# Kernel optimization log

Hardware: AMD Instinct MI355X
Metric: run time of the kernel (lower is better)

The kernel has to match this reference:

```python
import jax, jax.numpy as jnp
import numpy as np

# dims
B, FIN, FOUT = 4, 64, 32
FMID = min(FIN, FOUT)          # fmiddle
NCLS, NH = 4, 64               # num_classes, SPADE nhidden
S = 32                         # D = H = W
EPS = 1e-5


def conv3d(x, w, b=None, pad=1):
    # x: [N,C,D,H,W], w: [O,I,kd,kh,kw]
    out = jax.lax.conv_general_dilated(
        x, w, window_strides=(1, 1, 1), padding=[(pad, pad)] * 3,
        dimension_numbers=('NCDHW', 'OIDHW', 'NCDHW'))
    if b is not None:
        out = out + b[None, :, None, None, None]
    return out


def instance_norm(x):
    # per-sample, per-channel over spatial dims (InstanceNorm3d, affine=False)
    mu = x.mean(axis=(2, 3, 4), keepdims=True)
    var = x.var(axis=(2, 3, 4), keepdims=True)
    return (x - mu) * jax.lax.rsqrt(var + EPS)


def spade(x, y, Ws, Bs, Wg, Bg, Wb, Bb):
    # x: [B,C,D,H,W]; param stacks have leading num_classes dim; y routes per sample.
    normalized = instance_norm(x)
    ws, bs, wg, bg, wb, bb = Ws[y], Bs[y], Wg[y], Bg[y], Wb[y], Bb[y]

    def one(xi, wsi, bsi, wgi, bgi, wbi, bbi):
        xi = xi[None]  # [1,C,D,H,W]
        actv = jax.nn.relu(conv3d(xi, wsi, bsi))
        gamma = conv3d(actv, wgi, bgi)[0]
        beta = conv3d(actv, wbi, bbi)[0]
        return gamma, beta

    gamma, beta = jax.vmap(one)(x, ws, bs, wg, bg, wb, bb)
    return normalized * (1.0 + gamma) + beta


def _lrelu(t):
    return jax.nn.leaky_relu(t, 0.2)


def setup_inputs() -> dict:
    key = jax.random.key(0)
    ks = jax.random.split(key, 24)
    sc = 0.05
    inp = {
        'x': jax.random.normal(ks[0], (B, FIN, S, S, S), jnp.float32),
        'y': jax.random.randint(ks[1], (B,), 0, NCLS, jnp.int64
                                if jax.config.jax_enable_x64 else jnp.int32),
        # SPADE norm_0 stacks: label_nc = norm_nc = FIN
        's0_ws': jax.random.normal(ks[2], (NCLS, NH, FIN, 3, 3, 3), jnp.float32) * sc,
        's0_bs': jnp.zeros((NCLS, NH), jnp.float32),
        's0_wg': jax.random.normal(ks[3], (NCLS, FIN, NH, 3, 3, 3), jnp.float32) * sc,
        's0_bg': jnp.zeros((NCLS, FIN), jnp.float32),
        's0_wb': jax.random.normal(ks[4], (NCLS, FIN, NH, 3, 3, 3), jnp.float32) * sc,
        's0_bb': jnp.zeros((NCLS, FIN), jnp.float32),
        # SPADE norm_1 stacks: label_nc = norm_nc = FMID
        's1_ws': jax.random.normal(ks[5], (NCLS, NH, FMID, 3, 3, 3), jnp.float32) * sc,
        's1_bs': jnp.zeros((NCLS, NH), jnp.float32),
        's1_wg': jax.random.normal(ks[6], (NCLS, FMID, NH, 3, 3, 3), jnp.float32) * sc,
        's1_bg': jnp.zeros((NCLS, FMID), jnp.float32),
        's1_wb': jax.random.normal(ks[7], (NCLS, FMID, NH, 3, 3, 3), jnp.float32) * sc,
        's1_bb': jnp.zeros((NCLS, FMID), jnp.float32),
        # resnet convs
        'conv0_w': jax.random.normal(ks[8], (FMID, FIN, 3, 3, 3), jnp.float32) * sc,
        'conv0_b': jnp.zeros((FMID,), jnp.float32),
        'conv1_w': jax.random.normal(ks[9], (FOUT, FMID, 3, 3, 3), jnp.float32) * sc,
        'conv1_b': jnp.zeros((FOUT,), jnp.float32),
        'convs_w': jax.random.normal(ks[10], (FOUT, FIN, 1, 1, 1), jnp.float32) * sc,
    }
    return inp


def reference(x, y, s0_ws, s0_bs, s0_wg, s0_bg, s0_wb, s0_bb,
              s1_ws, s1_bs, s1_wg, s1_bg, s1_wb, s1_bb,
              conv0_w, conv0_b, conv1_w, conv1_b, convs_w):
    x_s = conv3d(x, convs_w, None, pad=0)  # learned shortcut (fin != fout, no bias)
    dx = conv3d(_lrelu(spade(x, y, s0_ws, s0_bs, s0_wg, s0_bg, s0_wb, s0_bb)),
                conv0_w, conv0_b)
    dx = conv3d(_lrelu(spade(dx, y, s1_ws, s1_bs, s1_wg, s1_bg, s1_wb, s1_bb)),
                conv1_w, conv1_b)
    return x_s + dx
```

## Files before the change

### kernel.cpp

```cpp
#include <hip/hip_runtime.h>


#define S3 32768
constexpr float EPS = 1e-5f;

typedef __attribute__((ext_vector_type(8))) short s16x8;
typedef __attribute__((ext_vector_type(4))) float f32x4;
typedef __attribute__((ext_vector_type(16))) float f32x16;
typedef __attribute__((ext_vector_type(4))) unsigned short u16x4;
typedef __attribute__((ext_vector_type(8))) unsigned short u16x8;

#define GLL(g, l)                                                        \
  __builtin_amdgcn_global_load_lds(                                      \
      (const __attribute__((address_space(1))) void*)(g),                \
      (__attribute__((address_space(3))) void*)(l), 16, 0, 0)

__device__ __forceinline__ float bf2f(unsigned short u) {
  union { unsigned int i; float f; } v; v.i = ((unsigned int)u) << 16; return v.f;
}
__device__ __forceinline__ unsigned short f2bf(float f) {
  union { float f; unsigned int i; } v; v.f = f;
  unsigned int r = (v.i + 0x7FFFu + ((v.i >> 16) & 1u)) >> 16;
  return (unsigned short)r;
}

__global__ __launch_bounds__(256) void stats_kernel(const float* __restrict__ x,
                                                    float* __restrict__ mu,
                                                    float* __restrict__ rstd) {
  const int bc = blockIdx.x;
  const float* p = x + (size_t)bc * S3;
  float s = 0.f, s2 = 0.f;
  for (int i = threadIdx.x; i < S3 / 4; i += 256) {
    float4 v = reinterpret_cast<const float4*>(p)[i];
    s  += v.x + v.y + v.z + v.w;
    s2 += v.x * v.x + v.y * v.y + v.z * v.z + v.w * v.w;
  }
  for (int off = 32; off; off >>= 1) {
    s  += __shfl_down(s, off, 64);
    s2 += __shfl_down(s2, off, 64);
  }
  __shared__ float ls[4], ls2[4];
  const int wid = threadIdx.x >> 6;
  if ((threadIdx.x & 63) == 0) { ls[wid] = s; ls2[wid] = s2; }
  __syncthreads();
  if (threadIdx.x == 0) {
    float S = 0.f, S2 = 0.f;
    for (int i = 0; i < 4; ++i) { S += ls[i]; S2 += ls2[i]; }
    const float m = S / (float)S3;
    const float var = S2 / (float)S3 - m * m;
    mu[bc] = m;
    rstd[bc] = rsqrtf(var + EPS);
  }
}

__global__ __launch_bounds__(256) void stats_t32_p1(const short* __restrict__ t,
                                                    float* __restrict__ part) {
  const int b = blockIdx.y;
  const int chunk = blockIdx.x;
  const int tid = threadIdx.x;
  const int pq = tid & 3;
  float s[8], s2[8];
#pragma unroll
  for (int j = 0; j < 8; ++j) { s[j] = 0.f; s2[j] = 0.f; }
  const int vbase = chunk * 512;
#pragma unroll
  for (int v = tid >> 2; v < 512; v += 64) {
    u16x8 u = *reinterpret_cast<const u16x8*>(
        &t[((size_t)b * S3 + vbase + v) * 32 + pq * 8]);
#pragma unroll
    for (int j = 0; j < 8; ++j) { float f = bf2f(u[j]); s[j] += f; s2[j] += f * f; }
  }
#pragma unroll
  for (int off = 4; off < 64; off <<= 1) {
#pragma unroll
    for (int j = 0; j < 8; ++j) {
      s[j]  += __shfl_xor(s[j], off, 64);
      s2[j] += __shfl_xor(s2[j], off, 64);
    }
  }
  __shared__ float red[4][4][16];
  const int wv = tid >> 6, lane = tid & 63;
  if (lane < 4) {
#pragma unroll
    for (int j = 0; j < 8; ++j) { red[wv][lane][j] = s[j]; red[wv][lane][8 + j] = s2[j]; }
  }
  __syncthreads();
  if (tid < 32) {
    const int p = tid >> 3, j = tid & 7;
    float S = 0.f, S2 = 0.f;
#pragma unroll
    for (int w = 0; w < 4; ++w) { S += red[w][p][j]; S2 += red[w][p][8 + j]; }
    const int c = p * 8 + j;
    part[((size_t)(b * 64 + chunk)) * 64 + c] = S;
    part[((size_t)(b * 64 + chunk)) * 64 + 32 + c] = S2;
  }
}

__global__ __launch_bounds__(128) void stats_t32_p2(const float* __restrict__ part,
                                                    float* __restrict__ mu,
                                                    float* __restrict__ rstd) {
  const int tid = threadIdx.x;
  const int b = tid >> 5, c = tid & 31;
  float S = 0.f, S2 = 0.f;
#pragma unroll 4
  for (int k = 0; k < 64; ++k) {
    S  += part[((size_t)(b * 64 + k)) * 64 + c];
    S2 += part[((size_t)(b * 64 + k)) * 64 + 32 + c];
  }
  const float m = S / (float)S3;
  const float var = S2 / (float)S3 - m * m;
  mu[b * 32 + c] = m;
  rstd[b * 32 + c] = rsqrtf(var + EPS);
}

__global__ __launch_bounds__(256) void transpose_x(const float* __restrict__ x,
                                                   short* __restrict__ xt) {
  const int b = blockIdx.y;
  const int v0 = blockIdx.x * 64;
  __shared__ unsigned short t[64][72];
  const int vox = threadIdx.x & 63;
  const int cg = threadIdx.x >> 6;
#pragma unroll
  for (int k = 0; k < 16; ++k) {
    const int ci = cg * 16 + k;
    t[vox][ci] = f2bf(x[((size_t)(b * 64 + ci)) * S3 + v0 + vox]);
  }
  __syncthreads();
  const int vv = threadIdx.x >> 2, part = threadIdx.x & 3;
  uint4 u0 = *reinterpret_cast<const uint4*>(&t[vv][part * 16]);
  uint4 u1 = *reinterpret_cast<const uint4*>(&t[vv][part * 16 + 8]);
  short* dst = &xt[((size_t)(b * S3 + v0 + vv)) * 64 + part * 16];
  *reinterpret_cast<uint4*>(dst) = u0;
  *reinterpret_cast<uint4*>(dst + 8) = u1;
}

__global__ __launch_bounds__(256) void repack_w(
    const float* __restrict__ wA, const float* __restrict__ wB,
    short* __restrict__ dst, const int* __restrict__ y,
    int CBLK, int CO2, int CI, long clsA, long clsB, int paired, int total) {
  const int b = blockIdx.y;
  const int idx = blockIdx.x * 256 + threadIdx.x;
  if (idx >= total) return;
  const int cls = y[b];
  const int KCH = CI / 16;
  const int ci = idx & 15;
  const int co = (idx >> 4) % CO2;
  const int rest = idx / (16 * CO2);
  const int k16 = rest % KCH;
  const int tap = rest / KCH;
  const int srcch = k16 * 16 + ci;
  float v;
  if (paired) {
    const int H = CBLK >> 1;
    const int blk = co / CBLK, w = co % CBLK;
    if (w < H)
      v = wA[(size_t)clsA * cls + ((size_t)(blk * H + w) * CI + srcch) * 27 + tap];
    else
      v = wB[(size_t)clsB * cls + ((size_t)(blk * H + w - H) * CI + srcch) * 27 + tap];
  } else {
    v = wA[(size_t)clsA * cls + ((size_t)co * CI + srcch) * 27 + tap];
  }
  dst[(((size_t)(b * 27 + tap) * KCH + k16) * CO2 + co) * 16 + ci] = (short)f2bf(v);
}

template <int CIN, int CBLK, int COTOT, int EPI, int NNORM>
__global__ __launch_bounds__(256, 2) void conv_mfma(
    const short* __restrict__ xt,
    const short* __restrict__ W,
    const float* __restrict__ bias,
    int bias_stride,
    const int* __restrict__ y,
    const short* __restrict__ xnb,
    const float* __restrict__ mu,
    const float* __restrict__ rstd,
    const float* __restrict__ bgs,
    const float* __restrict__ bbs,
    const short* __restrict__ zp,
    float* __restrict__ outf,
    short* __restrict__ outb) {
  constexpr int KCH = CIN / 16;
  constexpr int NCOG = CBLK / 32;
  constexpr int WIT = (CBLK == 64) ? 1280 : 768;
  constexpr int WSH = (CBLK == 64) ? 6 : 5;

  __shared__ short ldsX[2048 * 8];
  __shared__ short ldsW[WIT * 8];

  const int tid = threadIdx.x;
  const int lane = tid & 63, wid = tid >> 6;
  const int l31 = lane & 31, khf = lane >> 5;
  const int b = blockIdx.y;
  const int cls = y[b];
  const int co_base = blockIdx.z * CBLK;
  const int tile = blockIdx.x;
  const int d0 = (tile >> 4) * 8, h0 = ((tile >> 2) & 3) * 8, w0 = (tile & 3) * 8;

  const short* gsrc[8];
#pragma unroll
  for (int k = 0; k < 8; ++k) {
    const int i = tid + k * 256;
    const int slot = i >> 1, half = i & 1;
    const short* g = zp;
    if (slot < 1000) {
      const int pd = slot / 100, r0 = slot - pd * 100;
      const int ph = r0 / 10, pw = r0 - ph * 10;
      const int gd = d0 + pd - 1, gh = h0 + ph - 1, gw = w0 + pw - 1;
      if ((unsigned)gd < 32u && (unsigned)gh < 32u && (unsigned)gw < 32u)
        g = xt + ((size_t)b * S3 + gd * 1024 + gh * 32 + gw) * CIN + half * 8;
    }
    gsrc[k] = g;
  }

  f32x16 acc[4][NCOG];
#pragma unroll
  for (int v = 0; v < 4; ++v)
#pragma unroll
    for (int c = 0; c < NCOG; ++c)
#pragma unroll
      for (int r = 0; r < 16; ++r) acc[v][c][r] = 0.f;

  const int hw = (l31 >> 3) * 10 + (l31 & 7);

#pragma unroll 1
  for (int kc = 0; kc < KCH; ++kc) {
#pragma unroll 1
    for (int kd = 0; kd < 3; ++kd) {
#pragma unroll
      for (int k = 0; k < WIT / 256; ++k) {
        const int i = tid + k * 256;
        const int row = i >> 1, half = i & 1;
        const int t9 = row >> WSH;
        const int co = row & (CBLK - 1);
        const short* g = (t9 < 9)
            ? W + (((size_t)(b * 27 + kd * 9 + t9) * KCH + kc) * COTOT +
                   co_base + co) * 16 + half * 8
            : zp;
        GLL(g, &ldsW[i * 8]);
      }
      if (kd == 0) {
#pragma unroll
        for (int k = 0; k < 8; ++k) {
          const int i = tid + k * 256;
          GLL(gsrc[k] + kc * 16, &ldsX[i * 8]);
        }
      }
      __syncthreads();

#pragma unroll
      for (int kh = 0; kh < 3; ++kh) {
#pragma unroll
        for (int kw = 0; kw < 3; ++kw) {
          s16x8 af[NCOG];
#pragma unroll
          for (int c = 0; c < NCOG; ++c)
            af[c] = *reinterpret_cast<const s16x8*>(
                &ldsW[((kh * 3 + kw) * CBLK + c * 32 + l31) * 16 + khf * 8]);
          s16x8 bf[4];
#pragma unroll
          for (int vg = 0; vg < 4; ++vg) {
            const int slot = (2 * wid + (vg >> 1) + kd) * 100 +
                             ((vg & 1) * 4 + kh) * 10 + kw + hw;
            bf[vg] = *reinterpret_cast<const s16x8*>(&ldsX[slot * 16 + khf * 8]);
          }
#pragma unroll
          for (int c = 0; c < NCOG; ++c)
#pragma unroll
            for (int vg = 0; vg < 4; ++vg)
              acc[vg][c] = __builtin_amdgcn_mfma_f32_32x32x16_bf16(
                  af[c], bf[vg], acc[vg][c], 0, 0, 0);
        }
      }
      __syncthreads();
    }
  }

  const int vdb = d0 + 2 * wid;
  const int vhb = h0 + (l31 >> 3);
  const int vwb = w0 + (l31 & 7);

  if constexpr (EPI == 0 || EPI == 1) {
#pragma unroll
    for (int c = 0; c < NCOG; ++c)
#pragma unroll
      for (int q = 0; q < 4; ++q) {
        const int c0 = co_base + c * 32 + q * 8 + khf * 4;
        const f32x4 b4 = *reinterpret_cast<const f32x4*>(&bias[cls * bias_stride + c0]);
#pragma unroll
        for (int vg = 0; vg < 4; ++vg) {
          const int gv = (vdb + (vg >> 1)) * 1024 + (vhb + (vg & 1) * 4) * 32 + vwb;
          u16x4 o;
#pragma unroll
          for (int rr = 0; rr < 4; ++rr) {
            float v = acc[vg][c][q * 4 + rr] + b4[rr];
            if constexpr (EPI == 0) v = fmaxf(v, 0.f);
            o[rr] = f2bf(v);
          }
          *reinterpret_cast<u16x4*>(&outb[((size_t)b * S3 + gv) * COTOT + c0]) = o;
        }
      }
  }

  if constexpr (EPI == 2) {
    const int nb = blockIdx.z * 32;
#pragma unroll
    for (int q = 0; q < 4; ++q) {
      const int c0 = nb + q * 8 + khf * 4;
      const f32x4 m4  = *reinterpret_cast<const f32x4*>(&mu[b * NNORM + c0]);
      const f32x4 r4  = *reinterpret_cast<const f32x4*>(&rstd[b * NNORM + c0]);
      const f32x4 g4  = *reinterpret_cast<const f32x4*>(&bgs[cls * NNORM + c0]);
      const f32x4 bb4 = *reinterpret_cast<const f32x4*>(&bbs[cls * NNORM + c0]);
#pragma unroll
      for (int vg = 0; vg < 4; ++vg) {
        const int gv = (vdb + (vg >> 1)) * 1024 + (vhb + (vg & 1) * 4) * 32 + vwb;
        const size_t vgl = (size_t)b * S3 + gv;
        u16x4 u = *reinterpret_cast<const u16x4*>(&xnb[vgl * NNORM + c0]);
        u16x4 o;
#pragma unroll
        for (int rr = 0; rr < 4; ++rr) {
          const float gamma = acc[vg][0][q * 4 + rr] + g4[rr];
          const float beta  = acc[vg][1][q * 4 + rr] + bb4[rr];
          const float nrm = (bf2f(u[rr]) - m4[rr]) * r4[rr];
          float h = nrm * (1.f + gamma) + beta;
          h = h > 0.f ? h : 0.2f * h;
          o[rr] = f2bf(h);
        }
        *reinterpret_cast<u16x4*>(&outb[vgl * NNORM + c0]) = o;
      }
    }
  }

  if constexpr (EPI == 4) {
#pragma unroll
    for (int q = 0; q < 4; ++q) {
      const int c0 = q * 8 + khf * 4;
      const f32x4 b4 = *reinterpret_cast<const f32x4*>(&bias[c0]);
#pragma unroll
      for (int vg = 0; vg < 4; ++vg) {
        const int gv = (vdb + (vg >> 1)) * 1024 + (vhb + (vg & 1) * 4) * 32 + vwb;
#pragma unroll
        for (int rr = 0; rr < 4; ++rr) {
          float* p = &outf[((size_t)(b * 32 + c0 + rr)) * S3 + gv];
          *p += acc[vg][0][q * 4 + rr] + b4[rr];
        }
      }
    }
  }
}

__global__ __launch_bounds__(256) void shortcut_kernel(const float* __restrict__ x,
                                                       const float* __restrict__ wsc,
                                                       float* __restrict__ out) {
  const int b = blockIdx.y;
  const int v = blockIdx.x * 256 + threadIdx.x;
  __shared__ float lw[64 * 32];
  for (int i = threadIdx.x; i < 2048; i += 256) {
    int ci = i >> 5, o = i & 31;
    lw[i] = wsc[o * 64 + ci];
  }
  __syncthreads();
  float acc[32];
#pragma unroll
  for (int o = 0; o < 32; ++o) acc[o] = 0.f;
  const float* xp = x + (size_t)b * 64 * S3 + v;
#pragma unroll 1
  for (int ci = 0; ci < 64; ++ci) {
    const float xv = xp[(size_t)ci * S3];
    const float4* wp = reinterpret_cast<const float4*>(&lw[ci << 5]);
#pragma unroll
    for (int o4 = 0; o4 < 8; ++o4) {
      float4 w4 = wp[o4];
      acc[o4 * 4 + 0] += xv * w4.x;
      acc[o4 * 4 + 1] += xv * w4.y;
      acc[o4 * 4 + 2] += xv * w4.z;
      acc[o4 * 4 + 3] += xv * w4.w;
    }
  }
  float* op = out + (size_t)b * 32 * S3 + v;
#pragma unroll
  for (int o = 0; o < 32; ++o) op[(size_t)o * S3] = acc[o];
}

extern "C" void kernel_launch(void* const* d_in, const int* in_sizes, int n_in,
                              void* d_out, int out_size, void* d_ws, size_t ws_size,
                              hipStream_t stream) {
  const float* x       = (const float*)d_in[0];
  const int*   y       = (const int*)d_in[1];
  const float* s0_ws   = (const float*)d_in[2];
  const float* s0_bs   = (const float*)d_in[3];
  const float* s0_wg   = (const float*)d_in[4];
  const float* s0_bg   = (const float*)d_in[5];
  const float* s0_wb   = (const float*)d_in[6];
  const float* s0_bb   = (const float*)d_in[7];
  const float* s1_ws   = (const float*)d_in[8];
  const float* s1_bs   = (const float*)d_in[9];
  const float* s1_wg   = (const float*)d_in[10];
  const float* s1_bg   = (const float*)d_in[11];
  const float* s1_wb   = (const float*)d_in[12];
  const float* s1_bb   = (const float*)d_in[13];
  const float* conv0_w = (const float*)d_in[14];
  const float* conv0_b = (const float*)d_in[15];
  const float* conv1_w = (const float*)d_in[16];
  const float* conv1_b = (const float*)d_in[17];
  const float* convs_w = (const float*)d_in[18];

  float* out = (float*)d_out;
  char* ws = (char*)d_ws;
  short* xt    = (short*)(ws);
  short* actvT = (short*)(ws + 16777216);
  short* hT    = (short*)(ws + 33554432);
  short* d0T   = (short*)(ws + 50331648);
  short* Wa0   = (short*)(ws + 58720256);
  short* Ws0   = (short*)(ws + 60817408);
  short* Wc0   = (short*)(ws + 62914560);
  short* Wa1   = (short*)(ws + 65011712);
  short* Ws1   = (short*)(ws + 67108864);
  short* Wc1   = (short*)(ws + 69206016);
  short* zp    = (short*)(ws + 70254592);
  float* stats = (float*)(ws + 71303168);
  float* mu0 = stats, *rstd0 = stats + 256, *mu1 = stats + 512, *rstd1 = stats + 640;
  float* spart = stats + 1024;

  hipMemsetAsync(zp, 0, 4096, stream);

  transpose_x<<<dim3(512, 4), 256, 0, stream>>>(x, xt);
  stats_kernel<<<dim3(256), 256, 0, stream>>>(x, mu0, rstd0);

  repack_w<<<dim3(432, 4), 256, 0, stream>>>(s0_ws, nullptr, Wa0, y, 64, 64, 64,
                                             64L * 64 * 27, 0, 0, 110592);
  repack_w<<<dim3(864, 4), 256, 0, stream>>>(s0_wg, s0_wb, Ws0, y, 64, 128, 64,
                                             64L * 64 * 27, 64L * 64 * 27, 1, 221184);
  repack_w<<<dim3(216, 4), 256, 0, stream>>>(conv0_w, nullptr, Wc0, y, 32, 32, 64,
                                             0, 0, 0, 55296);
  repack_w<<<dim3(216, 4), 256, 0, stream>>>(s1_ws, nullptr, Wa1, y, 64, 64, 32,
                                             64L * 32 * 27, 0, 0, 55296);
  repack_w<<<dim3(432, 4), 256, 0, stream>>>(s1_wg, s1_wb, Ws1, y, 64, 64, 64,
                                             32L * 64 * 27, 32L * 64 * 27, 1, 110592);
  repack_w<<<dim3(108, 4), 256, 0, stream>>>(conv1_w, nullptr, Wc1, y, 32, 32, 32,
                                             0, 0, 0, 27648);

  conv_mfma<64, 64, 64, 0, 0><<<dim3(64, 4, 1), 256, 0, stream>>>(
      xt, Wa0, s0_bs, 64, y, nullptr, nullptr, nullptr, nullptr, nullptr, zp,
      nullptr, actvT);
  conv_mfma<64, 64, 128, 2, 64><<<dim3(64, 4, 2), 256, 0, stream>>>(
      actvT, Ws0, nullptr, 0, y, xt, mu0, rstd0, s0_bg, s0_bb, zp,
      nullptr, hT);
  conv_mfma<64, 32, 32, 1, 0><<<dim3(64, 4, 1), 256, 0, stream>>>(
      hT, Wc0, conv0_b, 0, y, nullptr, nullptr, nullptr, nullptr, nullptr, zp,
      nullptr, d0T);
  stats_t32_p1<<<dim3(64, 4), 256, 0, stream>>>(d0T, spart);
  stats_t32_p2<<<dim3(1), 128, 0, stream>>>(spart, mu1, rstd1);
  conv_mfma<32, 64, 64, 0, 0><<<dim3(64, 4, 1), 256, 0, stream>>>(
      d0T, Wa1, s1_bs, 64, y, nullptr, nullptr, nullptr, nullptr, nullptr, zp,
      nullptr, actvT);
  conv_mfma<64, 64, 64, 2, 32><<<dim3(64, 4, 1), 256, 0, stream>>>(
      actvT, Ws1, nullptr, 0, y, d0T, mu1, rstd1, s1_bg, s1_bb, zp,
      nullptr, hT);
  shortcut_kernel<<<dim3(128, 4), 256, 0, stream>>>(x, convs_w, out);
  conv_mfma<32, 32, 32, 4, 0><<<dim3(64, 4, 1), 256, 0, stream>>>(
      hT, Wc1, conv1_b, 0, y, nullptr, nullptr, nullptr, nullptr, nullptr, zp,
      out, nullptr);
}
```

Before: 303.1 us.

## Double-buffer LDS staging and halve spatial tile to double conv grid

The conv kernel now double-buffers both the weight and input tiles in LDS, issuing the next phase's global-to-LDS loads before computing the current one, with a single barrier per phase instead of two. The spatial tile shrinks from 8x8x8 to 4x8x8 voxels, so each wave handles 2 instead of 4 MFMA column groups and the grid doubles to 128 tiles per sample. The aim is to hide load latency and raise occupancy and parallelism across CUs. In exchange the input halo is re-fetched more often relative to the compute it feeds, and the doubled LDS footprint may limit how many blocks fit per CU.

```diff
diff --git a/kernel.cpp b/kernel.cpp
--- a/kernel.cpp
+++ b/kernel.cpp
@@ -180,11 +180,11 @@
     short* __restrict__ outb) {
   constexpr int KCH = CIN / 16;
   constexpr int NCOG = CBLK / 32;
-  constexpr int WIT = (CBLK == 64) ? 1280 : 768;
+  constexpr int WCH = 9 * CBLK * 2;
   constexpr int WSH = (CBLK == 64) ? 6 : 5;
 
-  __shared__ short ldsX[2048 * 8];
-  __shared__ short ldsW[WIT * 8];
+  __shared__ short ldsX[2][1200 * 8];
+  __shared__ short ldsW[2][WCH * 8];
 
   const int tid = threadIdx.x;
   const int lane = tid & 63, wid = tid >> 6;
@@ -193,90 +193,97 @@
   const int cls = y[b];
   const int co_base = blockIdx.z * CBLK;
   const int tile = blockIdx.x;
-  const int d0 = (tile >> 4) * 8, h0 = ((tile >> 2) & 3) * 8, w0 = (tile & 3) * 8;
-
-  const short* gsrc[8];
-#pragma unroll
-  for (int k = 0; k < 8; ++k) {
+  const int d0 = (tile >> 4) * 4, h0 = ((tile >> 2) & 3) * 8, w0 = (tile & 3) * 8;
+
+  const short* gsrc[5];
+#pragma unroll
+  for (int k = 0; k < 5; ++k) {
     const int i = tid + k * 256;
-    const int slot = i >> 1, half = i & 1;
     const short* g = zp;
-    if (slot < 1000) {
-      const int pd = slot / 100, r0 = slot - pd * 100;
-      const int ph = r0 / 10, pw = r0 - ph * 10;
-      const int gd = d0 + pd - 1, gh = h0 + ph - 1, gw = w0 + pw - 1;
+    if (i < 1200) {
+      const int slot = i >> 1, half = i & 1;
+      const int sd = slot / 100, r0 = slot - sd * 100;
+      const int sh = r0 / 10, sw = r0 - sh * 10;
+      const int gd = d0 + sd - 1, gh = h0 + sh - 1, gw = w0 + sw - 1;
       if ((unsigned)gd < 32u && (unsigned)gh < 32u && (unsigned)gw < 32u)
         g = xt + ((size_t)b * S3 + gd * 1024 + gh * 32 + gw) * CIN + half * 8;
     }
     gsrc[k] = g;
   }
 
-  f32x16 acc[4][NCOG];
-#pragma unroll
-  for (int v = 0; v < 4; ++v)
+  auto stage_x = [&](int kc, int xb) {
+#pragma unroll
+    for (int k = 0; k < 5; ++k) {
+      const int i = tid + k * 256;
+      if (i < 1200) GLL(gsrc[k] + kc * 16, &ldsX[xb][i * 8]);
+    }
+  };
+  auto stage_w = [&](int kc, int kd, int wb) {
+#pragma unroll
+    for (int k = 0; k < (WCH + 255) / 256; ++k) {
+      const int i = tid + k * 256;
+      if (i < WCH) {
+        const int row = i >> 1, half = i & 1;
+        const int t9 = row >> WSH, co = row & (CBLK - 1);
+        GLL(W + (((size_t)(b * 27 + kd * 9 + t9) * KCH + kc) * COTOT +
+                 co_base + co) * 16 + half * 8,
+            &ldsW[wb][i * 8]);
+      }
+    }
+  };
+
+  f32x16 acc[2][NCOG];
+#pragma unroll
+  for (int v = 0; v < 2; ++v)
 #pragma unroll
     for (int c = 0; c < NCOG; ++c)
 #pragma unroll
       for (int r = 0; r < 16; ++r) acc[v][c][r] = 0.f;
 
-  const int hw = (l31 >> 3) * 10 + (l31 & 7);
-
-#pragma unroll 1
-  for (int kc = 0; kc < KCH; ++kc) {
-#pragma unroll 1
-    for (int kd = 0; kd < 3; ++kd) {
-#pragma unroll
-      for (int k = 0; k < WIT / 256; ++k) {
-        const int i = tid + k * 256;
-        const int row = i >> 1, half = i & 1;
-        const int t9 = row >> WSH;
-        const int co = row & (CBLK - 1);
-        const short* g = (t9 < 9)
-            ? W + (((size_t)(b * 27 + kd * 9 + t9) * KCH + kc) * COTOT +
-                   co_base + co) * 16 + half * 8
-            : zp;
-        GLL(g, &ldsW[i * 8]);
+  const int hwb = ((l31 >> 3) * 10 + (l31 & 7)) * 16 + khf * 8;
+
+  stage_x(0, 0);
+  stage_w(0, 0, 0);
+  __syncthreads();
+
+  int xb = 0;
+#pragma unroll
+  for (int ph = 0; ph < KCH * 3; ++ph) {
+    const int kd = ph % 3;
+    const int wb = ph & 1;
+    if (ph + 1 < KCH * 3) {
+      const int nkc = (ph + 1) / 3, nkd = (ph + 1) % 3;
+      stage_w(nkc, nkd, wb ^ 1);
+      if (nkd == 0) stage_x(nkc, xb ^ 1);
+    }
+#pragma unroll
+    for (int kh = 0; kh < 3; ++kh) {
+#pragma unroll
+      for (int kw = 0; kw < 3; ++kw) {
+        s16x8 af[NCOG];
+#pragma unroll
+        for (int c = 0; c < NCOG; ++c)
+          af[c] = *reinterpret_cast<const s16x8*>(
+              &ldsW[wb][((kh * 3 + kw) * CBLK + c * 32 + l31) * 16 + khf * 8]);
+        s16x8 bf[2];
+#pragma unroll
+        for (int vg = 0; vg < 2; ++vg) {
+          const int so = ((wid + kd) * 100 + (vg * 4 + kh) * 10 + kw) * 16;
+          bf[vg] = *reinterpret_cast<const s16x8*>(&ldsX[xb][so + hwb]);
+        }
+#pragma unroll
+        for (int c = 0; c < NCOG; ++c)
+#pragma unroll
+          for (int vg = 0; vg < 2; ++vg)
+            acc[vg][c] = __builtin_amdgcn_mfma_f32_32x32x16_bf16(
+                af[c], bf[vg], acc[vg][c], 0, 0, 0);
       }
-      if (kd == 0) {
-#pragma unroll
-        for (int k = 0; k < 8; ++k) {
-          const int i = tid + k * 256;
-          GLL(gsrc[k] + kc * 16, &ldsX[i * 8]);
-        }
-      }
-      __syncthreads();
-
-#pragma unroll
-      for (int kh = 0; kh < 3; ++kh) {
-#pragma unroll
-        for (int kw = 0; kw < 3; ++kw) {
-          s16x8 af[NCOG];
-#pragma unroll
-          for (int c = 0; c < NCOG; ++c)
-            af[c] = *reinterpret_cast<const s16x8*>(
-                &ldsW[((kh * 3 + kw) * CBLK + c * 32 + l31) * 16 + khf * 8]);
-          s16x8 bf[4];
-#pragma unroll
-          for (int vg = 0; vg < 4; ++vg) {
-            const int slot = (2 * wid + (vg >> 1) + kd) * 100 +
-                             ((vg & 1) * 4 + kh) * 10 + kw + hw;
-            bf[vg] = *reinterpret_cast<const s16x8*>(&ldsX[slot * 16 + khf * 8]);
-          }
-#pragma unroll
-          for (int c = 0; c < NCOG; ++c)
-#pragma unroll
-            for (int vg = 0; vg < 4; ++vg)
-              acc[vg][c] = __builtin_amdgcn_mfma_f32_32x32x16_bf16(
-                  af[c], bf[vg], acc[vg][c], 0, 0, 0);
-        }
-      }
-      __syncthreads();
-    }
-  }
-
-  const int vdb = d0 + 2 * wid;
-  const int vhb = h0 + (l31 >> 3);
-  const int vwb = w0 + (l31 & 7);
+    }
+    __syncthreads();
+    if (kd == 2) xb ^= 1;
+  }
+
+  const int dgv = (d0 + wid) * 1024 + (h0 + (l31 >> 3)) * 32 + w0 + (l31 & 7);
 
   if constexpr (EPI == 0 || EPI == 1) {
 #pragma unroll
@@ -286,8 +293,8 @@
         const int c0 = co_base + c * 32 + q * 8 + khf * 4;
         const f32x4 b4 = *reinterpret_cast<const f32x4*>(&bias[cls * bias_stride + c0]);
 #pragma unroll
-        for (int vg = 0; vg < 4; ++vg) {
-          const int gv = (vdb + (vg >> 1)) * 1024 + (vhb + (vg & 1) * 4) * 32 + vwb;
+        for (int vg = 0; vg < 2; ++vg) {
+          const int gv = dgv + vg * 128;
           u16x4 o;
 #pragma unroll
           for (int rr = 0; rr < 4; ++rr) {
@@ -310,8 +317,8 @@
       const f32x4 g4  = *reinterpret_cast<const f32x4*>(&bgs[cls * NNORM + c0]);
       const f32x4 bb4 = *reinterpret_cast<const f32x4*>(&bbs[cls * NNORM + c0]);
 #pragma unroll
-      for (int vg = 0; vg < 4; ++vg) {
-        const int gv = (vdb + (vg >> 1)) * 1024 + (vhb + (vg & 1) * 4) * 32 + vwb;
+      for (int vg = 0; vg < 2; ++vg) {
+        const int gv = dgv + vg * 128;
         const size_t vgl = (size_t)b * S3 + gv;
         u16x4 u = *reinterpret_cast<const u16x4*>(&xnb[vgl * NNORM + c0]);
         u16x4 o;
@@ -335,8 +342,8 @@
       const int c0 = q * 8 + khf * 4;
       const f32x4 b4 = *reinterpret_cast<const f32x4*>(&bias[c0]);
 #pragma unroll
-      for (int vg = 0; vg < 4; ++vg) {
-        const int gv = (vdb + (vg >> 1)) * 1024 + (vhb + (vg & 1) * 4) * 32 + vwb;
+      for (int vg = 0; vg < 2; ++vg) {
+        const int gv = dgv + vg * 128;
 #pragma unroll
         for (int rr = 0; rr < 4; ++rr) {
           float* p = &outf[((size_t)(b * 32 + c0 + rr)) * S3 + gv];
@@ -438,25 +445,25 @@
   repack_w<<<dim3(108, 4), 256, 0, stream>>>(conv1_w, nullptr, Wc1, y, 32, 32, 32,
                                              0, 0, 0, 27648);
 
-  conv_mfma<64, 64, 64, 0, 0><<<dim3(64, 4, 1), 256, 0, stream>>>(
+  conv_mfma<64, 64, 64, 0, 0><<<dim3(128, 4, 1), 256, 0, stream>>>(
       xt, Wa0, s0_bs, 64, y, nullptr, nullptr, nullptr, nullptr, nullptr, zp,
       nullptr, actvT);
-  conv_mfma<64, 64, 128, 2, 64><<<dim3(64, 4, 2), 256, 0, stream>>>(
+  conv_mfma<64, 64, 128, 2, 64><<<dim3(128, 4, 2), 256, 0, stream>>>(
       actvT, Ws0, nullptr, 0, y, xt, mu0, rstd0, s0_bg, s0_bb, zp,
       nullptr, hT);
-  conv_mfma<64, 32, 32, 1, 0><<<dim3(64, 4, 1), 256, 0, stream>>>(
+  conv_mfma<64, 32, 32, 1, 0><<<dim3(128, 4, 1), 256, 0, stream>>>(
       hT, Wc0, conv0_b, 0, y, nullptr, nullptr, nullptr, nullptr, nullptr, zp,
       nullptr, d0T);
   stats_t32_p1<<<dim3(64, 4), 256, 0, stream>>>(d0T, spart);
   stats_t32_p2<<<dim3(1), 128, 0, stream>>>(spart, mu1, rstd1);
-  conv_mfma<32, 64, 64, 0, 0><<<dim3(64, 4, 1), 256, 0, stream>>>(
+  conv_mfma<32, 64, 64, 0, 0><<<dim3(128, 4, 1), 256, 0, stream>>>(
       d0T, Wa1, s1_bs, 64, y, nullptr, nullptr, nullptr, nullptr, nullptr, zp,
       nullptr, actvT);
-  conv_mfma<64, 64, 64, 2, 32><<<dim3(64, 4, 1), 256, 0, stream>>>(
+  conv_mfma<64, 64, 64, 2, 32><<<dim3(128, 4, 1), 256, 0, stream>>>(
       actvT, Ws1, nullptr, 0, y, d0T, mu1, rstd1, s1_bg, s1_bb, zp,
       nullptr, hT);
   shortcut_kernel<<<dim3(128, 4), 256, 0, stream>>>(x, convs_w, out);
-  conv_mfma<32, 32, 32, 4, 0><<<dim3(64, 4, 1), 256, 0, stream>>>(
+  conv_mfma<32, 32, 32, 4, 0><<<dim3(128, 4, 1), 256, 0, stream>>>(
       hT, Wc1, conv1_b, 0, y, nullptr, nullptr, nullptr, nullptr, nullptr, zp,
       out, nullptr);
 }
```

After: 301.8 us. Within noise of the previous version (-0.4%).

## Software-pipeline conv MFMA with triple-buffered weights and double-buffered input tiles

Applied to the files above, without the earlier changes.

Replaces the load-sync-compute-sync loop in the MFMA conv kernel with a fully unrolled pipeline. Weights are triple-buffered two phases ahead and input tiles are double-buffered one channel chunk ahead, with explicit vmcnt waits and a single barrier per phase. The LDS layouts are changed so each lane reads contiguous 8-element rows. MFMA priority is raised during compute. The larger LDS footprint drops launch bounds to one block per CU, trading occupancy for overlap of global loads with compute.

```diff
diff --git a/kernel.cpp b/kernel.cpp
--- a/kernel.cpp
+++ b/kernel.cpp
@@ -14,6 +14,11 @@
   __builtin_amdgcn_global_load_lds(                                      \
       (const __attribute__((address_space(1))) void*)(g),                \
       (__attribute__((address_space(3))) void*)(l), 16, 0, 0)
+
+template <int N>
+__device__ __forceinline__ void wait_vm() {
+  asm volatile("s_waitcnt vmcnt(%0)" ::"n"(N) : "memory");
+}
 
 __device__ __forceinline__ float bf2f(unsigned short u) {
   union { unsigned int i; float f; } v; v.i = ((unsigned int)u) << 16; return v.f;
@@ -164,7 +169,7 @@
 }
 
 template <int CIN, int CBLK, int COTOT, int EPI, int NNORM>
-__global__ __launch_bounds__(256, 2) void conv_mfma(
+__global__ __launch_bounds__(256, 1) void conv_mfma(
     const short* __restrict__ xt,
     const short* __restrict__ W,
     const float* __restrict__ bias,
@@ -179,12 +184,14 @@
     float* __restrict__ outf,
     short* __restrict__ outb) {
   constexpr int KCH = CIN / 16;
+  constexpr int NPH = 3 * KCH;
   constexpr int NCOG = CBLK / 32;
-  constexpr int WIT = (CBLK == 64) ? 1280 : 768;
-  constexpr int WSH = (CBLK == 64) ? 6 : 5;
-
-  __shared__ short ldsX[2048 * 8];
-  __shared__ short ldsW[WIT * 8];
+  constexpr int WGP = ((9 * NCOG * 64 + 255) / 256) * 256;
+  constexpr int WISS = WGP / 256;
+  constexpr int XISS = 8;
+
+  __shared__ short ldsX[2][2048 * 8];
+  __shared__ short ldsW[3][WGP * 8];
 
   const int tid = threadIdx.x;
   const int lane = tid & 63, wid = tid >> 6;
@@ -195,22 +202,48 @@
   const int tile = blockIdx.x;
   const int d0 = (tile >> 4) * 8, h0 = ((tile >> 2) & 3) * 8, w0 = (tile & 3) * 8;
 
-  const short* gsrc[8];
-#pragma unroll
-  for (int k = 0; k < 8; ++k) {
+  const short* gsrc[XISS];
+#pragma unroll
+  for (int k = 0; k < XISS; ++k) {
     const int i = tid + k * 256;
-    const int slot = i >> 1, half = i & 1;
+    const int pl = i >> 10, slot = i & 1023;
     const short* g = zp;
     if (slot < 1000) {
-      const int pd = slot / 100, r0 = slot - pd * 100;
-      const int ph = r0 / 10, pw = r0 - ph * 10;
-      const int gd = d0 + pd - 1, gh = h0 + ph - 1, gw = w0 + pw - 1;
+      const int sd = slot / 100, r0 = slot - sd * 100;
+      const int sh = r0 / 10, sw0 = r0 - sh * 10;
+      const int gd = d0 + sd - 1, gh = h0 + sh - 1, gw = w0 + sw0 - 1;
       if ((unsigned)gd < 32u && (unsigned)gh < 32u && (unsigned)gw < 32u)
-        g = xt + ((size_t)b * S3 + gd * 1024 + gh * 32 + gw) * CIN + half * 8;
+        g = xt + ((size_t)b * S3 + gd * 1024 + gh * 32 + gw) * CIN + pl * 8;
     }
     gsrc[k] = g;
   }
 
+  auto stage_x = [&](int kc, int xbuf) {
+    const bool real = kc < KCH;
+#pragma unroll
+    for (int k = 0; k < XISS; ++k) {
+      const int i = tid + k * 256;
+      GLL(real ? gsrc[k] + kc * 16 : zp, &ldsX[xbuf][i * 8]);
+    }
+  };
+  auto stage_w = [&](int ph, int wbuf) {
+    const bool real = ph < NPH;
+    const int kc = ph / 3, kd = ph % 3;
+#pragma unroll
+    for (int k = 0; k < WISS; ++k) {
+      const int i = tid + k * 256;
+      const short* g = zp;
+      if (real && i < 9 * NCOG * 64) {
+        const int t9 = i / (NCOG * 64);
+        const int r = i - t9 * (NCOG * 64);
+        const int c = r >> 6, q = r & 63;
+        g = W + (((size_t)(b * 27 + kd * 9 + t9) * KCH + kc) * COTOT +
+                 co_base + c * 32 + (q & 31)) * 16 + (q >> 5) * 8;
+      }
+      GLL(g, &ldsW[wbuf][i * 8]);
+    }
+  };
+
   f32x16 acc[4][NCOG];
 #pragma unroll
   for (int v = 0; v < 4; ++v)
@@ -219,60 +252,61 @@
 #pragma unroll
       for (int r = 0; r < 16; ++r) acc[v][c][r] = 0.f;
 
-  const int hw = (l31 >> 3) * 10 + (l31 & 7);
-
-#pragma unroll 1
-  for (int kc = 0; kc < KCH; ++kc) {
-#pragma unroll 1
-    for (int kd = 0; kd < 3; ++kd) {
-#pragma unroll
-      for (int k = 0; k < WIT / 256; ++k) {
-        const int i = tid + k * 256;
-        const int row = i >> 1, half = i & 1;
-        const int t9 = row >> WSH;
-        const int co = row & (CBLK - 1);
-        const short* g = (t9 < 9)
-            ? W + (((size_t)(b * 27 + kd * 9 + t9) * KCH + kc) * COTOT +
-                   co_base + co) * 16 + half * 8
-            : zp;
-        GLL(g, &ldsW[i * 8]);
+  const int hwoff = (l31 >> 3) * 10 + (l31 & 7);
+  const int xpl = khf * 1024;
+
+  stage_w(0, 0);
+  stage_x(0, 0);
+  stage_w(1, 1);
+  wait_vm<WISS>();
+  __builtin_amdgcn_sched_barrier(0);
+  __builtin_amdgcn_s_barrier();
+  __builtin_amdgcn_sched_barrier(0);
+
+#pragma unroll
+  for (int p = 0; p < NPH; ++p) {
+    const int kc = p / 3, kd = p % 3;
+    stage_w(p + 2, (p + 2) % 3);
+    if (kd == 0) stage_x(kc + 1, (kc + 1) & 1);
+
+    __builtin_amdgcn_s_setprio(1);
+#pragma unroll
+    for (int kh = 0; kh < 3; ++kh) {
+#pragma unroll
+      for (int kw = 0; kw < 3; ++kw) {
+        const int t9 = kh * 3 + kw;
+        s16x8 af[NCOG];
+#pragma unroll
+        for (int c = 0; c < NCOG; ++c)
+          af[c] = *reinterpret_cast<const s16x8*>(
+              &ldsW[p % 3][((t9 * NCOG + c) * 64 + lane) * 8]);
+        s16x8 bf[4];
+#pragma unroll
+        for (int vg = 0; vg < 4; ++vg) {
+          const int slot = (2 * wid + (vg >> 1) + kd) * 100 +
+                           ((vg & 1) * 4 + kh) * 10 + kw + hwoff;
+          bf[vg] = *reinterpret_cast<const s16x8*>(&ldsX[kc & 1][(xpl + slot) * 8]);
+        }
+#pragma unroll
+        for (int c = 0; c < NCOG; ++c)
+#pragma unroll
+          for (int vg = 0; vg < 4; ++vg)
+            acc[vg][c] = __builtin_amdgcn_mfma_f32_32x32x16_bf16(
+                af[c], bf[vg], acc[vg][c], 0, 0, 0);
       }
-      if (kd == 0) {
-#pragma unroll
-        for (int k = 0; k < 8; ++k) {
-          const int i = tid + k * 256;
-          GLL(gsrc[k] + kc * 16, &ldsX[i * 8]);
-        }
-      }
-      __syncthreads();
-
-#pragma unroll
-      for (int kh = 0; kh < 3; ++kh) {
-#pragma unroll
-        for (int kw = 0; kw < 3; ++kw) {
-          s16x8 af[NCOG];
-#pragma unroll
-          for (int c = 0; c < NCOG; ++c)
-            af[c] = *reinterpret_cast<const s16x8*>(
-                &ldsW[((kh * 3 + kw) * CBLK + c * 32 + l31) * 16 + khf * 8]);
-          s16x8 bf[4];
-#pragma unroll
-          for (int vg = 0; vg < 4; ++vg) {
-            const int slot = (2 * wid + (vg >> 1) + kd) * 100 +
-                             ((vg & 1) * 4 + kh) * 10 + kw + hw;
-            bf[vg] = *reinterpret_cast<const s16x8*>(&ldsX[slot * 16 + khf * 8]);
-          }
-#pragma unroll
-          for (int c = 0; c < NCOG; ++c)
-#pragma unroll
-            for (int vg = 0; vg < 4; ++vg)
-              acc[vg][c] = __builtin_amdgcn_mfma_f32_32x32x16_bf16(
-                  af[c], bf[vg], acc[vg][c], 0, 0, 0);
-        }
-      }
-      __syncthreads();
-    }
-  }
+    }
+    __builtin_amdgcn_s_setprio(0);
+
+    if (p < NPH - 1) {
+      if (p % 3 == 2) wait_vm<WISS>();
+      else            wait_vm<WISS + XISS>();
+      __builtin_amdgcn_sched_barrier(0);
+      __builtin_amdgcn_s_barrier();
+      __builtin_amdgcn_sched_barrier(0);
+    }
+  }
+  wait_vm<0>();
+  __builtin_amdgcn_sched_barrier(0);
 
   const int vdb = d0 + 2 * wid;
   const int vhb = h0 + (l31 >> 3);
```

Result: slower. 320.6 us (+5.8%).

## Split LDS operand layout into planar halves, swizzle tile order, raise MFMA priority

Applied to the files above, without the earlier changes.

The X tile in LDS now uses two planes, one per 8-channel half, and the W tile is stored in per-lane MFMA fragment order, so each lane's 16-byte LDS reads land on contiguous addresses and should see fewer bank conflicts. Block-to-tile mapping is transposed, which changes the order in which spatial tiles are scheduled, likely for L2 locality. The sync pattern changes to a barrier before staging plus one after, dropping the trailing barrier. s_setprio is raised around the MFMA loop. Together these aim to reduce LDS conflicts and improve issue, at the cost of somewhat more address arithmetic during staging.

```diff
diff --git a/kernel.cpp b/kernel.cpp
--- a/kernel.cpp
+++ b/kernel.cpp
@@ -180,11 +180,12 @@
     short* __restrict__ outb) {
   constexpr int KCH = CIN / 16;
   constexpr int NCOG = CBLK / 32;
-  constexpr int WIT = (CBLK == 64) ? 1280 : 768;
-  constexpr int WSH = (CBLK == 64) ? 6 : 5;
+  constexpr int WG = 9 * NCOG * 64;
+  constexpr int WGP = ((WG + 255) / 256) * 256;
+  constexpr int WISS = WGP / 256;
 
   __shared__ short ldsX[2048 * 8];
-  __shared__ short ldsW[WIT * 8];
+  __shared__ short ldsW[WGP * 8];
 
   const int tid = threadIdx.x;
   const int lane = tid & 63, wid = tid >> 6;
@@ -192,25 +193,48 @@
   const int b = blockIdx.y;
   const int cls = y[b];
   const int co_base = blockIdx.z * CBLK;
-  const int tile = blockIdx.x;
+  const int tile = (blockIdx.x & 7) * 8 + (blockIdx.x >> 3);
   const int d0 = (tile >> 4) * 8, h0 = ((tile >> 2) & 3) * 8, w0 = (tile & 3) * 8;
 
   const short* gsrc[8];
 #pragma unroll
   for (int k = 0; k < 8; ++k) {
     const int i = tid + k * 256;
-    const int slot = i >> 1, half = i & 1;
+    const int pl = i >> 10, slot = i & 1023;
     const short* g = zp;
     if (slot < 1000) {
-      const int pd = slot / 100, r0 = slot - pd * 100;
-      const int ph = r0 / 10, pw = r0 - ph * 10;
-      const int gd = d0 + pd - 1, gh = h0 + ph - 1, gw = w0 + pw - 1;
+      const int sd = slot / 100, r0 = slot - sd * 100;
+      const int sh = r0 / 10, sw0 = r0 - sh * 10;
+      const int gd = d0 + sd - 1, gh = h0 + sh - 1, gw = w0 + sw0 - 1;
       if ((unsigned)gd < 32u && (unsigned)gh < 32u && (unsigned)gw < 32u)
-        g = xt + ((size_t)b * S3 + gd * 1024 + gh * 32 + gw) * CIN + half * 8;
+        g = xt + ((size_t)b * S3 + gd * 1024 + gh * 32 + gw) * CIN + pl * 8;
     }
     gsrc[k] = g;
   }
 
+  auto stage_x = [&](int kc) {
+#pragma unroll
+    for (int k = 0; k < 8; ++k) {
+      const int i = tid + k * 256;
+      GLL(gsrc[k] + kc * 16, &ldsX[i * 8]);
+    }
+  };
+  auto stage_w = [&](int kc, int kd) {
+#pragma unroll
+    for (int k = 0; k < WISS; ++k) {
+      const int i = tid + k * 256;
+      const short* g = zp;
+      if (i < WG) {
+        const int t9 = i / (NCOG * 64);
+        const int r = i - t9 * (NCOG * 64);
+        const int c = r >> 6, q = r & 63;
+        g = W + (((size_t)(b * 27 + kd * 9 + t9) * KCH + kc) * COTOT +
+                 co_base + c * 32 + (q & 31)) * 16 + (q >> 5) * 8;
+      }
+      GLL(g, &ldsW[i * 8]);
+    }
+  };
+
   f32x16 acc[4][NCOG];
 #pragma unroll
   for (int v = 0; v < 4; ++v)
@@ -219,48 +243,35 @@
 #pragma unroll
       for (int r = 0; r < 16; ++r) acc[v][c][r] = 0.f;
 
-  const int hw = (l31 >> 3) * 10 + (l31 & 7);
+  const int hw10 = (l31 >> 3) * 10 + (l31 & 7);
+  const int xpl = khf * 1024;
 
 #pragma unroll 1
   for (int kc = 0; kc < KCH; ++kc) {
 #pragma unroll 1
     for (int kd = 0; kd < 3; ++kd) {
-#pragma unroll
-      for (int k = 0; k < WIT / 256; ++k) {
-        const int i = tid + k * 256;
-        const int row = i >> 1, half = i & 1;
-        const int t9 = row >> WSH;
-        const int co = row & (CBLK - 1);
-        const short* g = (t9 < 9)
-            ? W + (((size_t)(b * 27 + kd * 9 + t9) * KCH + kc) * COTOT +
-                   co_base + co) * 16 + half * 8
-            : zp;
-        GLL(g, &ldsW[i * 8]);
-      }
-      if (kd == 0) {
-#pragma unroll
-        for (int k = 0; k < 8; ++k) {
-          const int i = tid + k * 256;
-          GLL(gsrc[k] + kc * 16, &ldsX[i * 8]);
-        }
-      }
       __syncthreads();
-
+      stage_w(kc, kd);
+      if (kd == 0) stage_x(kc);
+      __syncthreads();
+
+      __builtin_amdgcn_s_setprio(1);
 #pragma unroll
       for (int kh = 0; kh < 3; ++kh) {
 #pragma unroll
         for (int kw = 0; kw < 3; ++kw) {
+          const int t9 = kh * 3 + kw;
           s16x8 af[NCOG];
 #pragma unroll
           for (int c = 0; c < NCOG; ++c)
             af[c] = *reinterpret_cast<const s16x8*>(
-                &ldsW[((kh * 3 + kw) * CBLK + c * 32 + l31) * 16 + khf * 8]);
+                &ldsW[((t9 * NCOG + c) * 64 + lane) * 8]);
           s16x8 bf[4];
 #pragma unroll
           for (int vg = 0; vg < 4; ++vg) {
             const int slot = (2 * wid + (vg >> 1) + kd) * 100 +
-                             ((vg & 1) * 4 + kh) * 10 + kw + hw;
-            bf[vg] = *reinterpret_cast<const s16x8*>(&ldsX[slot * 16 + khf * 8]);
+                             ((vg & 1) * 4 + kh) * 10 + kw + hw10;
+            bf[vg] = *reinterpret_cast<const s16x8*>(&ldsX[(xpl + slot) * 8]);
           }
 #pragma unroll
           for (int c = 0; c < NCOG; ++c)
@@ -270,7 +281,7 @@
                   af[c], bf[vg], acc[vg][c], 0, 0, 0);
         }
       }
-      __syncthreads();
+      __builtin_amdgcn_s_setprio(0);
     }
   }
 
```

Measured after the change: 284.8 us. -6.0%, faster.
